# Kernel tuning notes

Measured on AMD Instinct MI355X. Metric: run time of the kernel, lower is better.

Reference implementation:

```python
import jax, jax.numpy as jnp
import numpy as np

B, Q, K, D = 16, 2048, 2048, 512

def setup_inputs() -> dict:
    key = jax.random.key(0)
    k1, k2, k3 = jax.random.split(key, 3)
    query = jax.random.normal(k1, (B, Q, D), dtype=jnp.float32)
    values = jax.random.normal(k2, (B, K, D), dtype=jnp.float32)
    # nn.Linear(D, D, bias=False) weight, applied as values @ W.T
    W_attn = jax.random.normal(k3, (D, D), dtype=jnp.float32) * (1.0 / np.sqrt(D))
    return {"query": query, "values": values, "W_attn": W_attn}

def reference(query, values, W_attn):
    # keys = Linear(values) = values @ W_attn.T  -> [B, K, D]
    keys = jnp.einsum('bkd,ed->bke', values, W_attn)
    # scores[b,q,k] = query[b,q,:] . keys[b,k,:]
    scores = jnp.einsum('bqd,bkd->bqk', query, keys)
    attention_weights = jax.nn.softmax(scores, axis=-1)
    context = jnp.einsum('bqk,bkd->bqd', attention_weights, values)
    return (context, attention_weights)
```

## Files before the change

kernel.cpp:

```cpp
#include <hip/hip_runtime.h>


#define B_ 16
#define Q_ 2048
#define K_ 2048
#define D_ 512

typedef _Float16 half8  __attribute__((ext_vector_type(8)));
typedef _Float16 half4v __attribute__((ext_vector_type(4)));
typedef float    floatx4 __attribute__((ext_vector_type(4)));

__device__ __forceinline__ void gld16(const _Float16* g, _Float16* l) {
  __builtin_amdgcn_global_load_lds(
      (const __attribute__((address_space(1))) void*)g,
      (__attribute__((address_space(3))) void*)l, 16, 0, 0);
}


#define STAGE_A(DBUF, T, H)                                                    \
  { gld16(Ab + (long)(m0 + (H)*128 +      srow) * Kd + (T)*64 + scolsw,        \
          &As[DBUF][(H)*8192 +        wave*512]);                              \
    gld16(Ab + (long)(m0 + (H)*128 + 64 + srow) * Kd + (T)*64 + scolsw,        \
          &As[DBUF][(H)*8192 + 4096 + wave*512]); }

#define STAGE_B(DBUF, T, H)                                                    \
  { gld16(Bb + (long)(n0 + (H)*128 +      srow) * Kd + (T)*64 + scolsw,        \
          &Bs[DBUF][(H)*8192 +        wave*512]);                              \
    gld16(Bb + (long)(n0 + (H)*128 + 64 + srow) * Kd + (T)*64 + scolsw,        \
          &Bs[DBUF][(H)*8192 + 4096 + wave*512]); }

#define RD_A(DST, BUF, MH)                                                     \
  _Pragma("unroll") for (int mi = 0; mi < 4; ++mi)                             \
  _Pragma("unroll") for (int ks = 0; ks < 2; ++ks)                             \
    DST[mi][ks] = *(const half8*)(                                             \
        &As[BUF][(wm*128 + ((MH)*4 + mi)*16 + fr)*64 + ks*32 + fksw]);

#define RD_B(DST, BUF, NH)                                                     \
  _Pragma("unroll") for (int ni = 0; ni < 2; ++ni)                             \
  _Pragma("unroll") for (int ks = 0; ks < 2; ++ks)                             \
    DST[ni][ks] = *(const half8*)(                                             \
        &Bs[BUF][(wn*64 + ((NH)*2 + ni)*16 + fr)*64 + ks*32 + fksw]);

#define QUAD(AARR, BARR, MH, NH)                                               \
  _Pragma("unroll") for (int mi = 0; mi < 4; ++mi)                             \
  _Pragma("unroll") for (int ni = 0; ni < 2; ++ni)                             \
  _Pragma("unroll") for (int ks = 0; ks < 2; ++ks)                             \
    acc[(MH)*4 + mi][(NH)*2 + ni] = __builtin_amdgcn_mfma_f32_16x16x32_f16(    \
        AARR[mi][ks], BARR[ni][ks], acc[(MH)*4 + mi][(NH)*2 + ni], 0, 0, 0);

#define BAR_MID()                                                              \
  __builtin_amdgcn_s_barrier();                                                \
  asm volatile("s_waitcnt lgkmcnt(0)" ::: "memory");                           \
  __builtin_amdgcn_s_setprio(1);

#define BAR_END()                                                              \
  __builtin_amdgcn_s_setprio(0);                                               \
  __builtin_amdgcn_s_barrier();

template <bool OUT_HALF>
__global__ __launch_bounds__(512, 2)
void gemm256(const _Float16* __restrict__ A, const _Float16* __restrict__ Bm,
             void* __restrict__ Cv, int M, int N, int Kd,
             long sA, long sB, long sC)
{
  __shared__ _Float16 As[2][16384];
  __shared__ _Float16 Bs[2][16384];

  const int b = blockIdx.z;
  const _Float16* Ab = A + (long)b * sA;
  const _Float16* Bb = Bm + (long)b * sB;
  const int m0 = blockIdx.y * 256, n0 = blockIdx.x * 256;
  (void)M;

  const int tid = threadIdx.x, wave = tid >> 6, lane = tid & 63;
  const int wm = wave >> 2, wn = wave & 3;

  const int srow = tid >> 3;
  const int scolsw = ((tid & 7) * 8) ^ (((tid >> 5) & 1) << 4);
  const int fr = lane & 15;
  const int fksw = ((lane >> 4) * 8) ^ (((fr >> 2) & 1) << 4);

  floatx4 acc[8][4] = {};

  STAGE_A(0, 0, 0) STAGE_A(0, 0, 1) STAGE_B(0, 0, 0) STAGE_B(0, 0, 1)
  STAGE_A(1, 1, 0) STAGE_A(1, 1, 1)
  asm volatile("s_waitcnt vmcnt(4)" ::: "memory");
  __builtin_amdgcn_s_barrier();

  const int NI = Kd >> 7;
  for (int j = 0; j < NI; ++j) {
    const int E = 2 * j, O = E + 1;
    const bool ns = (j + 1 < NI);
    half8 aL[4][2], aH[4][2], bL[2][2], bH[2][2];

    RD_A(aL, 0, 0) RD_B(bL, 0, 0)
    STAGE_B(1, O, 0)
    BAR_MID() QUAD(aL, bL, 0, 0) BAR_END()

    RD_A(aH, 0, 1) RD_B(bH, 0, 1)
    STAGE_B(1, O, 1)
    BAR_MID() QUAD(aL, bH, 0, 1) BAR_END()

    if (ns) STAGE_A(0, E + 2, 0)
    BAR_MID() QUAD(aH, bH, 1, 1) BAR_END()

    if (ns) { STAGE_A(0, E + 2, 1)
              asm volatile("s_waitcnt vmcnt(4)" ::: "memory"); }
    else    { asm volatile("s_waitcnt vmcnt(0)" ::: "memory"); }
    BAR_MID() QUAD(aH, bL, 1, 0) BAR_END()

    RD_A(aL, 1, 0) RD_B(bL, 1, 0)
    if (ns) STAGE_B(0, E + 2, 0)
    BAR_MID() QUAD(aL, bL, 0, 0) BAR_END()

    RD_A(aH, 1, 1) RD_B(bH, 1, 1)
    if (ns) STAGE_B(0, E + 2, 1)
    BAR_MID() QUAD(aL, bH, 0, 1) BAR_END()

    if (ns) STAGE_A(1, O + 2, 0)
    BAR_MID() QUAD(aH, bH, 1, 1) BAR_END()

    if (ns) { STAGE_A(1, O + 2, 1)
              asm volatile("s_waitcnt vmcnt(4)" ::: "memory"); }
    BAR_MID() QUAD(aH, bL, 1, 0) BAR_END()
  }

  const int orow = (lane >> 4) * 4, ocol = lane & 15;
  if constexpr (OUT_HALF) {
    _Float16* Cp = (_Float16*)Cv + (long)b * sC;
#pragma unroll
    for (int mt = 0; mt < 8; ++mt)
#pragma unroll
      for (int nt = 0; nt < 4; ++nt)
#pragma unroll
        for (int r = 0; r < 4; ++r)
          Cp[(long)(m0 + wm*128 + mt*16 + orow + r) * N + (n0 + wn*64 + nt*16 + ocol)] =
              (_Float16)acc[mt][nt][r];
  } else {
    float* Cp = (float*)Cv + (long)b * sC;
#pragma unroll
    for (int mt = 0; mt < 8; ++mt)
#pragma unroll
      for (int nt = 0; nt < 4; ++nt)
#pragma unroll
        for (int r = 0; r < 4; ++r)
          Cp[(long)(m0 + wm*128 + mt*16 + orow + r) * N + (n0 + wn*64 + nt*16 + ocol)] =
              acc[mt][nt][r];
  }
}

__global__ __launch_bounds__(256)
void softmax_rows(float* __restrict__ S, _Float16* __restrict__ P)
{
  float* p = S + (long)blockIdx.x * 2048;
  const int tid = threadIdx.x, lane = tid & 63, wave = tid >> 6;

  float4 v0 = *(const float4*)(p + tid * 4);
  float4 v1 = *(const float4*)(p + 1024 + tid * 4);

  float mx = fmaxf(fmaxf(fmaxf(v0.x, v0.y), fmaxf(v0.z, v0.w)),
                   fmaxf(fmaxf(v1.x, v1.y), fmaxf(v1.z, v1.w)));
#pragma unroll
  for (int off = 32; off; off >>= 1) mx = fmaxf(mx, __shfl_down(mx, off, 64));

  __shared__ float red[8];
  if (lane == 0) red[wave] = mx;
  __syncthreads();
  mx = fmaxf(fmaxf(red[0], red[1]), fmaxf(red[2], red[3]));

  v0.x = __expf(v0.x - mx); v0.y = __expf(v0.y - mx);
  v0.z = __expf(v0.z - mx); v0.w = __expf(v0.w - mx);
  v1.x = __expf(v1.x - mx); v1.y = __expf(v1.y - mx);
  v1.z = __expf(v1.z - mx); v1.w = __expf(v1.w - mx);

  float s = v0.x + v0.y + v0.z + v0.w + v1.x + v1.y + v1.z + v1.w;
#pragma unroll
  for (int off = 32; off; off >>= 1) s += __shfl_down(s, off, 64);
  if (lane == 0) red[4 + wave] = s;
  __syncthreads();
  s = red[4] + red[5] + red[6] + red[7];

  float inv = 1.0f / s;
  v0.x *= inv; v0.y *= inv; v0.z *= inv; v0.w *= inv;
  v1.x *= inv; v1.y *= inv; v1.z *= inv; v1.w *= inv;
  *(float4*)(p + tid * 4) = v0;
  *(float4*)(p + 1024 + tid * 4) = v1;

  _Float16* ph = P + (long)blockIdx.x * 2048;
  half4v h0, h1;
  h0[0] = (_Float16)v0.x; h0[1] = (_Float16)v0.y;
  h0[2] = (_Float16)v0.z; h0[3] = (_Float16)v0.w;
  h1[0] = (_Float16)v1.x; h1[1] = (_Float16)v1.y;
  h1[2] = (_Float16)v1.z; h1[3] = (_Float16)v1.w;
  *(half4v*)(ph + tid * 4) = h0;
  *(half4v*)(ph + 1024 + tid * 4) = h1;
}

__global__ __launch_bounds__(256)
void convert_q(const float4* __restrict__ q, half4v* __restrict__ qh)
{
  long i = (long)blockIdx.x * 256 + threadIdx.x;
  float4 a = q[i];
  half4v h;
  h[0] = (_Float16)a.x; h[1] = (_Float16)a.y; h[2] = (_Float16)a.z; h[3] = (_Float16)a.w;
  qh[i] = h;
}

__global__ __launch_bounds__(256)
void transpose_v(const float* __restrict__ v, _Float16* __restrict__ vt,
                 _Float16* __restrict__ vh)
{
  __shared__ float tile[32][33];
  const int b = blockIdx.z, kk = blockIdx.y * 32, ee = blockIdx.x * 32;
  const float* vp = v + (long)b * K_ * D_;
  _Float16* vtp = vt + (long)b * D_ * K_;
  _Float16* vhp = vh + (long)b * K_ * D_;
  const int tx = threadIdx.x & 31, ty = threadIdx.x >> 5;
#pragma unroll
  for (int i = 0; i < 32; i += 8) {
    float x = vp[(long)(kk + ty + i) * D_ + ee + tx];
    tile[ty + i][tx] = x;
    vhp[(long)(kk + ty + i) * D_ + ee + tx] = (_Float16)x;
  }
  __syncthreads();
#pragma unroll
  for (int i = 0; i < 32; i += 8)
    vtp[(long)(ee + ty + i) * K_ + kk + tx] = (_Float16)tile[tx][ty + i];
}

extern "C" void kernel_launch(void* const* d_in, const int* in_sizes, int n_in,
                              void* d_out, int out_size, void* d_ws, size_t ws_size,
                              hipStream_t stream)
{
  const float* q = (const float*)d_in[0];
  const float* v = (const float*)d_in[1];
  const float* w = (const float*)d_in[2];

  float* ctx    = (float*)d_out;
  float* scores = ctx + (long)B_ * Q_ * D_;

  const long nQD = (long)B_ * Q_ * D_;
  const long nKD = (long)B_ * K_ * D_;
  const long nDK = (long)B_ * D_ * K_;
  const long nQK = (long)B_ * Q_ * K_;

  _Float16* wh  = (_Float16*)d_ws;
  _Float16* vth = wh + 512 * 512;
  _Float16* ph  = vth + nDK;
  _Float16* qh  = ph;
  _Float16* kh  = qh + nQD;
  _Float16* vh  = kh + nKD;
  (void)ws_size;

  convert_q<<<16384, 256, 0, stream>>>((const float4*)q, (half4v*)qh);
  convert_q<<<256,   256, 0, stream>>>((const float4*)w, (half4v*)wh);
  transpose_v<<<dim3(D_ / 32, K_ / 32, B_), 256, 0, stream>>>(v, vth, vh);

  gemm256<true><<<dim3(D_ / 256, K_ / 256, B_), 512, 0, stream>>>(
      vh, wh, kh, K_, D_, D_, (long)K_ * D_, 0l, (long)K_ * D_);

  gemm256<false><<<dim3(K_ / 256, Q_ / 256, B_), 512, 0, stream>>>(
      qh, kh, scores, Q_, K_, D_, (long)Q_ * D_, (long)K_ * D_, (long)Q_ * K_);

  softmax_rows<<<B_ * Q_, 256, 0, stream>>>(scores, ph);

  gemm256<false><<<dim3(D_ / 256, Q_ / 256, B_), 512, 0, stream>>>(
      ph, vth, ctx, Q_, D_, K_, (long)Q_ * K_, (long)D_ * K_, (long)Q_ * D_);
}
```

Measured before the change: 778.1 us.

## Use full XOR swizzle for GEMM LDS tiles and restructure prefetch schedule

Changes the LDS swizzle from a single-bit XOR to a full 3-bit row XOR across the 8 16-byte column chunks, which is meant to remove bank conflicts on the fragment reads. It also reorders the double-buffered global-to-LDS staging so both A and B of the next tile are prefetched earlier, splits the fragment reads across more phases, and deepens the vmcnt wait threshold. The intent is more overlap of memory loads with MFMA work, at the cost of more outstanding loads and a more delicate buffer-hazard schedule.

```diff
diff --git a/kernel.cpp b/kernel.cpp
--- a/kernel.cpp
+++ b/kernel.cpp
@@ -33,13 +33,13 @@
   _Pragma("unroll") for (int mi = 0; mi < 4; ++mi)                             \
   _Pragma("unroll") for (int ks = 0; ks < 2; ++ks)                             \
     DST[mi][ks] = *(const half8*)(                                             \
-        &As[BUF][(wm*128 + ((MH)*4 + mi)*16 + fr)*64 + ks*32 + fksw]);
+        &As[BUF][(wm*128 + ((MH)*4 + mi)*16 + fr)*64 + (fkxs ^ (ks << 5))]);
 
 #define RD_B(DST, BUF, NH)                                                     \
   _Pragma("unroll") for (int ni = 0; ni < 2; ++ni)                             \
   _Pragma("unroll") for (int ks = 0; ks < 2; ++ks)                             \
     DST[ni][ks] = *(const half8*)(                                             \
-        &Bs[BUF][(wn*64 + ((NH)*2 + ni)*16 + fr)*64 + ks*32 + fksw]);
+        &Bs[BUF][(wn*64 + ((NH)*2 + ni)*16 + fr)*64 + (fkxs ^ (ks << 5))]);
 
 #define QUAD(AARR, BARR, MH, NH)                                               \
   _Pragma("unroll") for (int mi = 0; mi < 4; ++mi)                             \
@@ -76,52 +76,53 @@
   const int wm = wave >> 2, wn = wave & 3;
 
   const int srow = tid >> 3;
-  const int scolsw = ((tid & 7) * 8) ^ (((tid >> 5) & 1) << 4);
+  const int scolsw = (((tid & 7) ^ ((tid >> 3) & 7)) << 3);
   const int fr = lane & 15;
-  const int fksw = ((lane >> 4) * 8) ^ (((fr >> 2) & 1) << 4);
+  const int fkxs = ((lane >> 4) * 8) ^ ((fr & 7) << 3);
 
   floatx4 acc[8][4] = {};
 
   STAGE_A(0, 0, 0) STAGE_A(0, 0, 1) STAGE_B(0, 0, 0) STAGE_B(0, 0, 1)
-  STAGE_A(1, 1, 0) STAGE_A(1, 1, 1)
-  asm volatile("s_waitcnt vmcnt(4)" ::: "memory");
+  STAGE_B(1, 1, 0) STAGE_B(1, 1, 1) STAGE_A(1, 1, 0) STAGE_A(1, 1, 1)
+  asm volatile("s_waitcnt vmcnt(8)" ::: "memory");
   __builtin_amdgcn_s_barrier();
 
   const int NI = Kd >> 7;
   for (int j = 0; j < NI; ++j) {
-    const int E = 2 * j, O = E + 1;
+    const int E2 = 2 * j + 2, O2 = 2 * j + 3;
     const bool ns = (j + 1 < NI);
     half8 aL[4][2], aH[4][2], bL[2][2], bH[2][2];
 
     RD_A(aL, 0, 0) RD_B(bL, 0, 0)
-    STAGE_B(1, O, 0)
     BAR_MID() QUAD(aL, bL, 0, 0) BAR_END()
 
-    RD_A(aH, 0, 1) RD_B(bH, 0, 1)
-    STAGE_B(1, O, 1)
+    RD_B(bH, 0, 1)
     BAR_MID() QUAD(aL, bH, 0, 1) BAR_END()
 
-    if (ns) STAGE_A(0, E + 2, 0)
+    RD_A(aH, 0, 1)
+    if (ns) STAGE_B(0, E2, 0)
     BAR_MID() QUAD(aH, bH, 1, 1) BAR_END()
 
-    if (ns) { STAGE_A(0, E + 2, 1)
+    if (ns) { STAGE_B(0, E2, 1)
               asm volatile("s_waitcnt vmcnt(4)" ::: "memory"); }
     else    { asm volatile("s_waitcnt vmcnt(0)" ::: "memory"); }
     BAR_MID() QUAD(aH, bL, 1, 0) BAR_END()
 
     RD_A(aL, 1, 0) RD_B(bL, 1, 0)
-    if (ns) STAGE_B(0, E + 2, 0)
+    if (ns) STAGE_A(0, E2, 0)
     BAR_MID() QUAD(aL, bL, 0, 0) BAR_END()
 
-    RD_A(aH, 1, 1) RD_B(bH, 1, 1)
-    if (ns) STAGE_B(0, E + 2, 1)
+    RD_B(bH, 1, 1)
+    if (ns) STAGE_A(0, E2, 1)
     BAR_MID() QUAD(aL, bH, 0, 1) BAR_END()
 
-    if (ns) STAGE_A(1, O + 2, 0)
+    RD_A(aH, 1, 1)
+    if (ns) STAGE_B(1, O2, 0)
     BAR_MID() QUAD(aH, bH, 1, 1) BAR_END()
 
-    if (ns) { STAGE_A(1, O + 2, 1)
-              asm volatile("s_waitcnt vmcnt(4)" ::: "memory"); }
+    if (ns) { STAGE_B(1, O2, 1)
+              STAGE_A(1, O2, 0) STAGE_A(1, O2, 1)
+              asm volatile("s_waitcnt vmcnt(8)" ::: "memory"); }
     BAR_MID() QUAD(aH, bL, 1, 0) BAR_END()
   }
 
@@ -242,7 +243,6 @@
   const long nQD = (long)B_ * Q_ * D_;
   const long nKD = (long)B_ * K_ * D_;
   const long nDK = (long)B_ * D_ * K_;
-  const long nQK = (long)B_ * Q_ * K_;
 
   _Float16* wh  = (_Float16*)d_ws;
   _Float16* vth = wh + 512 * 512;
```

New measurement: 757.8 us. 2.6% less time.
